# Performance work log

Measured on AMD Instinct MI355X. Metric: run time of the kernel, lower is better.

The kernel has to match this reference:

```python
import jax, jax.numpy as jnp
import numpy as np

N, E, D, L, H = 10000, 160000, 128, 3, 8
DH = D // H
EPS = 1e-5


def ln(x, g, b):
    m = x.mean(-1, keepdims=True)
    v = ((x - m) ** 2).mean(-1, keepdims=True)
    return (x - m) * jax.lax.rsqrt(v + EPS) * g + b


def setup_inputs() -> dict:
    key = jax.random.key(0)
    ks = iter(jax.random.split(key, 16))
    rn = lambda s, sc=0.05: jax.random.normal(next(ks), s, dtype=jnp.float32) * sc
    return {
        'lane_feats': jax.random.normal(next(ks), (N, 10), dtype=jnp.float32),
        'edge_attrs': jax.random.normal(next(ks), (E, 9), dtype=jnp.float32),
        'edge_index': jax.random.randint(next(ks), (2, E), 0, N),
        'node_W': rn((10, D)), 'node_b': jnp.zeros((D,)), 'node_g': jnp.ones((D,)), 'node_bt': jnp.zeros((D,)),
        'rpe_W': rn((9, D)), 'rpe_b': jnp.zeros((D,)), 'rpe_g': jnp.ones((D,)), 'rpe_bt': jnp.zeros((D,)),
        'mem_W': rn((L, 3 * D, D)), 'mem_b': jnp.zeros((L, D)), 'mem_g': jnp.ones((L, D)), 'mem_bt': jnp.zeros((L, D)),
        'Wq': rn((L, D, D)), 'Wk': rn((L, D, D)), 'Wv': rn((L, D, D)), 'Wo': rn((L, D, D)),
        'eu_W': rn((L, D, D)), 'eu_b': jnp.zeros((L, D)), 'eu_g': jnp.ones((L, D)), 'eu_bt': jnp.zeros((L, D)),
        'en_g': jnp.ones((L, D)), 'en_bt': jnp.zeros((L, D)),
        'ffn_W1': rn((L, D, 2 * D)), 'ffn_b1': jnp.zeros((L, 2 * D)),
        'ffn_W2': rn((L, 2 * D, D)), 'ffn_b2': jnp.zeros((L, D)),
        'n1_g': jnp.ones((L, D)), 'n1_bt': jnp.zeros((L, D)),
        'n2_g': jnp.ones((L, D)), 'n2_bt': jnp.zeros((L, D)),
    }


def reference(lane_feats, edge_attrs, edge_index,
              node_W, node_b, node_g, node_bt,
              rpe_W, rpe_b, rpe_g, rpe_bt,
              mem_W, mem_b, mem_g, mem_bt,
              Wq, Wk, Wv, Wo,
              eu_W, eu_b, eu_g, eu_bt,
              en_g, en_bt,
              ffn_W1, ffn_b1, ffn_W2, ffn_b2,
              n1_g, n1_bt, n2_g, n2_bt):
    src, dst = edge_index[0], edge_index[1]
    # input projections (dropout is identity in eval)
    x = jax.nn.relu(ln(lane_feats @ node_W + node_b, node_g, node_bt))  # [N, D]
    e = jax.nn.relu(ln(edge_attrs @ rpe_W + rpe_b, rpe_g, rpe_bt))      # [E, D]
    for l in range(L):
        x_i, x_j = x[dst], x[src]  # receiver / sender features [E, D]
        mem = jax.nn.relu(ln(jnp.concatenate([x_i, x_j, e], axis=-1) @ mem_W[l] + mem_b[l],
                             mem_g[l], mem_bt[l]))
        delta = jax.nn.relu(ln(mem @ eu_W[l] + eu_b[l], eu_g[l], eu_bt[l]))
        e = ln(e + delta, en_g[l], en_bt[l])
        q = (x_i @ Wq[l]).reshape(E, H, DH)
        k = (mem @ Wk[l]).reshape(E, H, DH)
        v = (mem @ Wv[l]).reshape(E, H, DH)
        logits = (q * k).sum(-1) / np.float32(np.sqrt(DH))  # [E, H]
        # segment softmax over destination nodes (pyg_softmax)
        mx = jax.ops.segment_max(logits, dst, num_segments=N)
        ex = jnp.exp(logits - mx[dst])
        sm = jax.ops.segment_sum(ex, dst, num_segments=N)
        attn = ex / (sm[dst] + 1e-16)
        out_e = (attn[..., None] * v).reshape(E, D) @ Wo[l]
        agg = jax.ops.segment_sum(out_e, dst, num_segments=N)  # scatter-add aggregation
        x = ln(x + agg, n1_g[l], n1_bt[l])
        h = jax.nn.relu(x @ ffn_W1[l] + ffn_b1[l]) @ ffn_W2[l] + ffn_b2[l]
        x = ln(x + h, n2_g[l], n2_bt[l])
    return x
```

## Files before the change

### kernel.cpp

```cpp
#include <hip/hip_runtime.h>
#include <cstdint>

#define NN 10000
#define NE 160000
#define DD 128
#define NL 3

typedef __attribute__((ext_vector_type(8))) __bf16 bf16x8;
typedef __attribute__((ext_vector_type(4))) float f32x4;

__device__ __forceinline__ ushort f2bf(float f) {
  unsigned u = __float_as_uint(f);
  return (ushort)((u + 0x7fffu + ((u >> 16) & 1u)) >> 16);
}
__device__ __forceinline__ float bf2f(ushort s) {
  return __uint_as_float(((unsigned)s) << 16);
}
__device__ __forceinline__ float wsum32(float v) {
  v += __shfl_xor(v, 1); v += __shfl_xor(v, 2); v += __shfl_xor(v, 4);
  v += __shfl_xor(v, 8); v += __shfl_xor(v, 16);
  return v;
}
__device__ __forceinline__ float wsum64(float v) {
  v = wsum32(v); v += __shfl_xor(v, 32); return v;
}
__device__ __forceinline__ void red16_2(float& a, float& b) {
#pragma unroll
  for (int m = 1; m < 16; m <<= 1) { a += __shfl_xor(a, m); b += __shfl_xor(b, m); }
}
__device__ __forceinline__ uint4 ldg16(const ushort* p) { return *(const uint4*)p; }

#define PH(id, MAXID, AT, ASTR, KK, AS) {                                       \
    if ((id) < (MAXID)) {                                                       \
      ushort* _db = Bb[((id) + 1) & 1];                                         \
      if ((id) & 1) { *(uint4*)(_db + tid * 8) = sa0;                           \
                      *(uint4*)(_db + 2048 + tid * 8) = sa1; }                  \
      else          { *(uint4*)(_db + tid * 8) = sb0;                           \
                      *(uint4*)(_db + 2048 + tid * 8) = sb1; }                  \
    }                                                                           \
    if ((id) + 2 <= (MAXID)) {                                                  \
      if ((id) & 1) { sb0 = ldg16(csrc((id) + 2, tid));                         \
                      sb1 = ldg16(csrc((id) + 2, 256 + tid)); }                 \
      else          { sa0 = ldg16(csrc((id) + 2, tid));                         \
                      sa1 = ldg16(csrc((id) + 2, 256 + tid)); }                 \
    }                                                                           \
    { bf16x8 _a = *(const bf16x8*)((AT) + (r0 + c) * (ASTR) + (KK) * 32 + g * 8); \
      const ushort* _bp = Bb[(id) & 1] + lane * 8;                              \
      _Pragma("unroll") for (int _t = 0; _t < 8; ++_t)                          \
        AS[_t] = __builtin_amdgcn_mfma_f32_16x16x32_bf16(                       \
            _a, *(const bf16x8*)(_bp + _t * 512), AS[_t], 0, 0, 0); }           \
    __syncthreads(); }

__global__ __launch_bounds__(256) void k_hist(const int* __restrict__ dst,
                                              int* __restrict__ deg) {
  int e = blockIdx.x * 256 + threadIdx.x;
  if (e < NE) atomicAdd(&deg[dst[e]], 1);
}

__global__ __launch_bounds__(256) void k_scan(const int* __restrict__ deg,
                                              int* __restrict__ rowptr,
                                              int* __restrict__ cursor) {
  __shared__ int part[256];
  const int t = threadIdx.x;
  const int CH = 40;
  int base = t * CH;
  int s = 0;
  for (int i = 0; i < CH; ++i) {
    int idx = base + i;
    s += (idx < NN) ? deg[idx] : 0;
  }
  part[t] = s;
  __syncthreads();
  for (int off = 1; off < 256; off <<= 1) {
    int v = (t >= off) ? part[t - off] : 0;
    __syncthreads();
    part[t] += v;
    __syncthreads();
  }
  int run = (t == 0) ? 0 : part[t - 1];
  for (int i = 0; i < CH; ++i) {
    int idx = base + i;
    if (idx < NN) {
      rowptr[idx] = run;
      cursor[idx] = run;
      run += deg[idx];
    }
  }
  if (t == 255) rowptr[NN] = part[255];
}

__global__ __launch_bounds__(256) void k_scatter(const int* __restrict__ dst,
                                                 int* __restrict__ cursor,
                                                 int* __restrict__ eids) {
  int e = blockIdx.x * 256 + threadIdx.x;
  if (e < NE) {
    int pos = atomicAdd(&cursor[dst[e]], 1);
    eids[pos] = e;
  }
}

__global__ __launch_bounds__(256) void k_permidx(const int* __restrict__ ei,
                                                 const int* __restrict__ perm,
                                                 int* __restrict__ srcP,
                                                 int* __restrict__ dstP) {
  int i = blockIdx.x * 256 + threadIdx.x;
  if (i < NE) {
    int e = perm[i];
    srcP[i] = ei[e];
    dstP[i] = ei[NE + e];
  }
}

__global__ __launch_bounds__(256) void k_transp(const float* __restrict__ in,
                                                ushort* __restrict__ out,
                                                int K, int N) {
  __shared__ float T[32][33];
  int k0 = blockIdx.x * 32, n0 = blockIdx.y * 32;
  in += (size_t)blockIdx.z * K * N;
  out += (size_t)blockIdx.z * K * N;
  int tx = threadIdx.x & 31, ty = threadIdx.x >> 5;
#pragma unroll
  for (int r = 0; r < 32; r += 8)
    if (k0 + ty + r < K && n0 + tx < N)
      T[ty + r][tx] = in[(size_t)(k0 + ty + r) * N + n0 + tx];
  __syncthreads();
#pragma unroll
  for (int r = 0; r < 32; r += 8)
    if (n0 + ty + r < N && k0 + tx < K)
      out[(size_t)(n0 + ty + r) * K + k0 + tx] = f2bf(T[tx][ty + r]);
}

template <int K>
__global__ __launch_bounds__(256) void k_inproj(
    const float* __restrict__ inp, const int* __restrict__ perm,
    const float* __restrict__ W, const float* __restrict__ b,
    const float* __restrict__ g, const float* __restrict__ bt,
    float* __restrict__ outF, ushort* __restrict__ outB, int rows) {
  int row = blockIdx.x * 4 + (threadIdx.x >> 6);
  if (row >= rows) return;
  int srow = perm ? perm[row] : row;
  int lane = threadIdx.x & 63;
  float a0 = b[lane], a1 = b[lane + 64];
#pragma unroll
  for (int k = 0; k < K; ++k) {
    float xv = inp[(size_t)srow * K + k];
    a0 = fmaf(xv, W[k * DD + lane], a0);
    a1 = fmaf(xv, W[k * DD + lane + 64], a1);
  }
  float m = wsum64(a0 + a1) * (1.0f / DD);
  float q = wsum64(a0 * a0 + a1 * a1) * (1.0f / DD);
  float rstd = rsqrtf(q - m * m + 1e-5f);
  float o0 = fmaxf((a0 - m) * rstd * g[lane] + bt[lane], 0.0f);
  float o1 = fmaxf((a1 - m) * rstd * g[lane + 64] + bt[lane + 64], 0.0f);
  size_t base = (size_t)row * DD;
  if (outF) { outF[base + lane] = o0; outF[base + lane + 64] = o1; }
  outB[base + lane] = f2bf(o0);
  outB[base + lane + 64] = f2bf(o1);
}

__global__ __launch_bounds__(256) void k_nodepre(
    const ushort* __restrict__ xb, const ushort* __restrict__ memWT,
    const ushort* __restrict__ WqT, const float* __restrict__ memB,
    float* __restrict__ Pa, float* __restrict__ Pb, ushort* __restrict__ qbo) {
  __shared__ __align__(16) ushort Xt[64 * 136];
  __shared__ __align__(16) ushort Bb[4096];
  const int tid = threadIdx.x;
  const int n0 = blockIdx.x * 64;
  const int z = blockIdx.y;
  const ushort* B0 = (z == 0) ? memWT : ((z == 1) ? memWT + 128 : WqT);
  const int bstr = (z < 2) ? 384 : 128;
  uint4 w[2], wn[2];
#pragma unroll
  for (int i = 0; i < 2; ++i) {
    int u = tid + i * 256;
    w[i] = ldg16(B0 + (size_t)(u >> 2) * bstr + (u & 3) * 8);
  }
#pragma unroll
  for (int it = 0; it < 4; ++it) {
    int ch = it * 256 + tid, row = ch >> 4, j = ch & 15;
    int gr = n0 + row; if (gr > NN - 1) gr = NN - 1;
    *(uint4*)(Xt + row * 136 + j * 8) = *(const uint4*)(xb + (size_t)gr * DD + j * 8);
  }
  const int lane = tid & 63, wv = tid >> 6;
  const int c = lane & 15, g = lane >> 4, r0 = wv * 16;
  f32x4 acc[8];
#pragma unroll
  for (int t = 0; t < 8; ++t) acc[t] = (f32x4){0.f, 0.f, 0.f, 0.f};
#pragma unroll
  for (int kk = 0; kk < 4; ++kk) {
    __syncthreads();
#pragma unroll
    for (int i = 0; i < 2; ++i) *(uint4*)(Bb + (tid + i * 256) * 8) = w[i];
    if (kk < 3) {
#pragma unroll
      for (int i = 0; i < 2; ++i) {
        int u = tid + i * 256;
        wn[i] = ldg16(B0 + (size_t)(u >> 2) * bstr + (kk + 1) * 32 + (u & 3) * 8);
      }
    }
    __syncthreads();
    bf16x8 a = *(const bf16x8*)(Xt + (r0 + c) * 136 + kk * 32 + g * 8);
#pragma unroll
    for (int t = 0; t < 8; ++t)
      acc[t] = __builtin_amdgcn_mfma_f32_16x16x32_bf16(
          a, *(const bf16x8*)(Bb + (t * 16 + c) * 32 + g * 8), acc[t], 0, 0, 0);
#pragma unroll
    for (int i = 0; i < 2; ++i) w[i] = wn[i];
  }
  if (z == 0) {
#pragma unroll
    for (int t = 0; t < 8; ++t) {
      float bv = memB[t * 16 + c];
#pragma unroll
      for (int rr = 0; rr < 4; ++rr) {
        int row = n0 + r0 + g * 4 + rr;
        if (row < NN) Pa[(size_t)row * DD + t * 16 + c] = acc[t][rr] + bv;
      }
    }
  } else if (z == 1) {
#pragma unroll
    for (int t = 0; t < 8; ++t)
#pragma unroll
      for (int rr = 0; rr < 4; ++rr) {
        int row = n0 + r0 + g * 4 + rr;
        if (row < NN) Pb[(size_t)row * DD + t * 16 + c] = acc[t][rr];
      }
  } else {
#pragma unroll
    for (int t = 0; t < 8; ++t)
#pragma unroll
      for (int rr = 0; rr < 4; ++rr) {
        int row = n0 + r0 + g * 4 + rr;
        if (row < NN) qbo[(size_t)row * DD + t * 16 + c] = f2bf(acc[t][rr]);
      }
  }
}

__global__ __launch_bounds__(256, 3) void k_edge(
    ushort* __restrict__ ebg, ushort* __restrict__ vbg,
    const float* __restrict__ Pa, const float* __restrict__ Pb,
    const ushort* __restrict__ qb, const int* __restrict__ srcP,
    const int* __restrict__ dstP, const ushort* __restrict__ memWT,
    const float* __restrict__ memG, const float* __restrict__ memBt,
    const ushort* __restrict__ euWT, const float* __restrict__ euB,
    const float* __restrict__ euG, const float* __restrict__ euBt,
    const float* __restrict__ enG, const float* __restrict__ enBt,
    const ushort* __restrict__ WkT, const ushort* __restrict__ WvT,
    float* __restrict__ lg) {
  __shared__ __align__(16) ushort Et[64 * 136];
  __shared__ __align__(16) ushort Mt[64 * 136];
  __shared__ __align__(16) ushort Bb[2][4096];
  const int tid = threadIdx.x;
  const int e0 = blockIdx.x * 64;
  const int lane = tid & 63, wv = tid >> 6;
  const int c = lane & 15, g = lane >> 4, r0 = wv * 16;

  auto csrc = [&](int j, int u) -> const ushort* {
    const ushort* base; int stride, off, kk = j & 3;
    if (j < 4)       { base = memWT; stride = 384; off = 256 + kk * 32; }
    else if (j < 8)  { base = euWT;  stride = 128; off = kk * 32; }
    else if (j < 12) { base = WkT;   stride = 128; off = kk * 32; }
    else             { base = WvT;   stride = 128; off = kk * 32; }
    return base + ((u >> 6) * 16 + (u & 15)) * stride + off + ((u >> 4) & 3) * 8;
  };

  int dv[4], sv[4];
#pragma unroll
  for (int rr = 0; rr < 4; ++rr) {
    int row = e0 + r0 + g * 4 + rr;
    dv[rr] = dstP[row]; sv[rr] = srcP[row];
  }
  uint4 sa0 = ldg16(csrc(0, tid)), sa1 = ldg16(csrc(0, 256 + tid));
  uint4 sb0 = ldg16(csrc(1, tid)), sb1 = ldg16(csrc(1, 256 + tid));
#pragma unroll
  for (int it = 0; it < 4; ++it) {
    int ch = it * 256 + tid, row = ch >> 4, j = ch & 15;
    *(uint4*)(Et + row * 136 + j * 8) =
        *(const uint4*)(ebg + (size_t)(e0 + row) * DD + j * 8);
  }
  *(uint4*)(Bb[0] + tid * 8) = sa0;
  *(uint4*)(Bb[0] + 2048 + tid * 8) = sa1;
  __syncthreads();

  f32x4 acc[8];

#pragma unroll
  for (int t = 0; t < 8; ++t) acc[t] = (f32x4){0.f, 0.f, 0.f, 0.f};
  PH(0, 15, Et, 136, 0, acc)
  PH(1, 15, Et, 136, 1, acc)
  PH(2, 15, Et, 136, 2, acc)
  PH(3, 15, Et, 136, 3, acc)

  {
    float ps[8][4];
#pragma unroll
    for (int t = 0; t < 8; ++t)
#pragma unroll
      for (int rr = 0; rr < 4; ++rr)
        ps[t][rr] = Pa[(size_t)dv[rr] * DD + t * 16 + c] +
                    Pb[(size_t)sv[rr] * DD + t * 16 + c];
    float s1[4] = {0, 0, 0, 0}, s2[4] = {0, 0, 0, 0};
#pragma unroll
    for (int t = 0; t < 8; ++t)
#pragma unroll
      for (int rr = 0; rr < 4; ++rr) {
        float s = acc[t][rr] + ps[t][rr];
        acc[t][rr] = s; s1[rr] += s; s2[rr] += s * s;
      }
    float mean[4], rstd[4];
#pragma unroll
    for (int rr = 0; rr < 4; ++rr) {
      red16_2(s1[rr], s2[rr]);
      mean[rr] = s1[rr] * (1.f / DD);
      rstd[rr] = rsqrtf(s2[rr] * (1.f / DD) - mean[rr] * mean[rr] + 1e-5f);
    }
#pragma unroll
    for (int t = 0; t < 8; ++t) {
      float gv = memG[t * 16 + c], tv = memBt[t * 16 + c];
#pragma unroll
      for (int rr = 0; rr < 4; ++rr) {
        float o = fmaxf((acc[t][rr] - mean[rr]) * rstd[rr] * gv + tv, 0.f);
        Mt[(r0 + g * 4 + rr) * 136 + t * 16 + c] = f2bf(o);
      }
    }
  }
  __syncthreads();

#pragma unroll
  for (int t = 0; t < 8; ++t) acc[t] = (f32x4){0.f, 0.f, 0.f, 0.f};
  PH(4, 15, Mt, 136, 0, acc)
  PH(5, 15, Mt, 136, 1, acc)
  PH(6, 15, Mt, 136, 2, acc)
  PH(7, 15, Mt, 136, 3, acc)

  {
    float s1[4] = {0, 0, 0, 0}, s2[4] = {0, 0, 0, 0};
#pragma unroll
    for (int t = 0; t < 8; ++t) {
      float bv = euB[t * 16 + c];
#pragma unroll
      for (int rr = 0; rr < 4; ++rr) {
        float v2 = acc[t][rr] + bv;
        acc[t][rr] = v2; s1[rr] += v2; s2[rr] += v2 * v2;
      }
    }
    float mean[4], rstd[4];
#pragma unroll
    for (int rr = 0; rr < 4; ++rr) {
      red16_2(s1[rr], s2[rr]);
      mean[rr] = s1[rr] * (1.f / DD);
      rstd[rr] = rsqrtf(s2[rr] * (1.f / DD) - mean[rr] * mean[rr] + 1e-5f);
    }
    float t1[4] = {0, 0, 0, 0}, t2[4] = {0, 0, 0, 0};
#pragma unroll
    for (int t = 0; t < 8; ++t) {
      float gv = euG[t * 16 + c], tv = euBt[t * 16 + c];
#pragma unroll
      for (int rr = 0; rr < 4; ++rr) {
        float d = fmaxf((acc[t][rr] - mean[rr]) * rstd[rr] * gv + tv, 0.f);
        float eo = bf2f(Et[(r0 + g * 4 + rr) * 136 + t * 16 + c]);
        float pv = eo + d;
        acc[t][rr] = pv; t1[rr] += pv; t2[rr] += pv * pv;
      }
    }
    float mean3[4], rstd3[4];
#pragma unroll
    for (int rr = 0; rr < 4; ++rr) {
      red16_2(t1[rr], t2[rr]);
      mean3[rr] = t1[rr] * (1.f / DD);
      rstd3[rr] = rsqrtf(t2[rr] * (1.f / DD) - mean3[rr] * mean3[rr] + 1e-5f);
    }
#pragma unroll
    for (int t = 0; t < 8; ++t) {
      float gv = enG[t * 16 + c], tv = enBt[t * 16 + c];
#pragma unroll
      for (int rr = 0; rr < 4; ++rr) {
        float en = (acc[t][rr] - mean3[rr]) * rstd3[rr] * gv + tv;
        Et[(r0 + g * 4 + rr) * 136 + t * 16 + c] = f2bf(en);
      }
    }
  }
  __syncthreads();
#pragma unroll
  for (int it = 0; it < 4; ++it) {
    int ch = it * 256 + tid, row = ch >> 4, j = ch & 15;
    *(uint4*)(ebg + (size_t)(e0 + row) * DD + j * 8) =
        *(const uint4*)(Et + row * 136 + j * 8);
  }

  float qvf[8][4];
#pragma unroll
  for (int t = 0; t < 8; ++t)
#pragma unroll
    for (int rr = 0; rr < 4; ++rr)
      qvf[t][rr] = bf2f(qb[(size_t)dv[rr] * DD + t * 16 + c]);

#pragma unroll
  for (int t = 0; t < 8; ++t) acc[t] = (f32x4){0.f, 0.f, 0.f, 0.f};
  PH(8, 15, Mt, 136, 0, acc)
  PH(9, 15, Mt, 136, 1, acc)
  PH(10, 15, Mt, 136, 2, acc)
  PH(11, 15, Mt, 136, 3, acc)
#pragma unroll
  for (int t = 0; t < 8; ++t) {
    float p[4];
#pragma unroll
    for (int rr = 0; rr < 4; ++rr) p[rr] = acc[t][rr] * qvf[t][rr];
#pragma unroll
    for (int m = 1; m < 16; m <<= 1)
#pragma unroll
      for (int rr = 0; rr < 4; ++rr) p[rr] += __shfl_xor(p[rr], m);
    if (c == t) {
#pragma unroll
      for (int rr = 0; rr < 4; ++rr)
        lg[(size_t)(e0 + r0 + g * 4 + rr) * 8 + t] = p[rr] * 0.25f;
    }
  }

#pragma unroll
  for (int t = 0; t < 8; ++t) acc[t] = (f32x4){0.f, 0.f, 0.f, 0.f};
  PH(12, 15, Mt, 136, 0, acc)
  PH(13, 15, Mt, 136, 1, acc)
  PH(14, 15, Mt, 136, 2, acc)
  PH(15, 15, Mt, 136, 3, acc)
#pragma unroll
  for (int t = 0; t < 8; ++t)
#pragma unroll
    for (int rr = 0; rr < 4; ++rr)
      Et[(r0 + g * 4 + rr) * 136 + t * 16 + c] = f2bf(acc[t][rr]);
  __syncthreads();
#pragma unroll
  for (int it = 0; it < 4; ++it) {
    int ch = it * 256 + tid, row = ch >> 4, j = ch & 15;
    *(uint4*)(vbg + (size_t)(e0 + row) * DD + j * 8) =
        *(const uint4*)(Et + row * 136 + j * 8);
  }
}

__global__ __launch_bounds__(256) void k_aggr(
    const ushort* __restrict__ vbg, const float* __restrict__ lg,
    const int* __restrict__ rowptr, float* __restrict__ agg) {
  int node = blockIdx.x * 4 + (threadIdx.x >> 6);
  if (node >= NN) return;
  const int lane = threadIdx.x & 63;
  const int j = lane & 7, h = lane >> 3;
  const int beg = rowptr[node], end = rowptr[node + 1];
  float mx = -3.4e38f;
  for (int i = beg + j; i < end; i += 8)
    mx = fmaxf(mx, lg[(size_t)i * 8 + h]);
  mx = fmaxf(mx, __shfl_xor(mx, 1));
  mx = fmaxf(mx, __shfl_xor(mx, 2));
  mx = fmaxf(mx, __shfl_xor(mx, 4));
  float sm = 0.f;
  for (int i = beg + j; i < end; i += 8)
    sm += expf(lg[(size_t)i * 8 + h] - mx);
  sm += __shfl_xor(sm, 1);
  sm += __shfl_xor(sm, 2);
  sm += __shfl_xor(sm, 4);
  float inv = 1.f / (sm + 1e-16f);
  float acc0 = 0.f, acc1 = 0.f;
  for (int i = beg; i < end; ++i) {
    float w = expf(lg[(size_t)i * 8 + h] - mx) * inv;
    ushort2 vv = *(const ushort2*)(vbg + (size_t)i * DD + lane * 2);
    acc0 = fmaf(bf2f(vv.x), w, acc0);
    acc1 = fmaf(bf2f(vv.y), w, acc1);
  }
  *(float2*)(agg + (size_t)node * DD + lane * 2) = make_float2(acc0, acc1);
}

__global__ __launch_bounds__(256) void k_node2(
    const float* __restrict__ vagg, const ushort* __restrict__ WoT,
    const float* __restrict__ xres_g, const float* __restrict__ g1,
    const float* __restrict__ bt1, const ushort* __restrict__ W1T,
    const float* __restrict__ b1, const ushort* __restrict__ W2T,
    const float* __restrict__ b2, const float* __restrict__ g2,
    const float* __restrict__ bt2, float* __restrict__ out,
    ushort* __restrict__ outB) {
  __shared__ __align__(16) ushort Xt[64 * 136];
  __shared__ __align__(16) ushort Hs[64 * 264];
  __shared__ __align__(16) ushort Bb[8192];
  const int tid = threadIdx.x;
  const int n0 = blockIdx.x * 64;
  const int lane = tid & 63, wv = tid >> 6;
  const int c = lane & 15, g = lane >> 4, r0 = wv * 16;

  float xres[8][4];
#pragma unroll
  for (int t = 0; t < 8; ++t)
#pragma unroll
    for (int rr = 0; rr < 4; ++rr) {
      int row = n0 + r0 + g * 4 + rr;
      if (row > NN - 1) row = NN - 1;
      xres[t][rr] = xres_g[(size_t)row * DD + t * 16 + c];
    }
  uint4 w[4], wn[4];
#pragma unroll
  for (int i = 0; i < 2; ++i) {
    int u = tid + i * 256;
    w[i] = ldg16(WoT + (size_t)(u >> 2) * 128 + (u & 3) * 8);
  }
#pragma unroll
  for (int it = 0; it < 8; ++it) {
    int ch = it * 256 + tid, row = ch >> 5, j = ch & 31;
    int gr = n0 + row; if (gr > NN - 1) gr = NN - 1;
    float4 vv = *(const float4*)(vagg + (size_t)gr * DD + j * 4);
    ushort4 ov; ov.x = f2bf(vv.x); ov.y = f2bf(vv.y); ov.z = f2bf(vv.z); ov.w = f2bf(vv.w);
    *(ushort4*)(Xt + row * 136 + j * 4) = ov;
  }
  f32x4 acc0[8];
#pragma unroll
  for (int t = 0; t < 8; ++t) acc0[t] = (f32x4){0.f, 0.f, 0.f, 0.f};
#pragma unroll
  for (int kk = 0; kk < 4; ++kk) {
    __syncthreads();
#pragma unroll
    for (int i = 0; i < 2; ++i) *(uint4*)(Bb + (tid + i * 256) * 8) = w[i];
    if (kk < 3) {
#pragma unroll
      for (int i = 0; i < 2; ++i) {
        int u = tid + i * 256;
        wn[i] = ldg16(WoT + (size_t)(u >> 2) * 128 + (kk + 1) * 32 + (u & 3) * 8);
      }
    }
    __syncthreads();
    bf16x8 a = *(const bf16x8*)(Xt + (r0 + c) * 136 + kk * 32 + g * 8);
#pragma unroll
    for (int t = 0; t < 8; ++t)
      acc0[t] = __builtin_amdgcn_mfma_f32_16x16x32_bf16(
          a, *(const bf16x8*)(Bb + (t * 16 + c) * 32 + g * 8), acc0[t], 0, 0, 0);
#pragma unroll
    for (int i = 0; i < 2; ++i) w[i] = wn[i];
  }
  {
    float s1[4] = {0, 0, 0, 0}, s2[4] = {0, 0, 0, 0};
#pragma unroll
    for (int t = 0; t < 8; ++t)
#pragma unroll
      for (int rr = 0; rr < 4; ++rr) {
        float s = acc0[t][rr] + xres[t][rr];
        acc0[t][rr] = s; s1[rr] += s; s2[rr] += s * s;
      }
    float mean[4], rstd[4];
#pragma unroll
    for (int rr = 0; rr < 4; ++rr) {
      red16_2(s1[rr], s2[rr]);
      mean[rr] = s1[rr] * (1.f / DD);
      rstd[rr] = rsqrtf(s2[rr] * (1.f / DD) - mean[rr] * mean[rr] + 1e-5f);
    }
#pragma unroll
    for (int t = 0; t < 8; ++t) {
      float gv = g1[t * 16 + c], tv = bt1[t * 16 + c];
#pragma unroll
      for (int rr = 0; rr < 4; ++rr) {
        float o = (acc0[t][rr] - mean[rr]) * rstd[rr] * gv + tv;
        Xt[(r0 + g * 4 + rr) * 136 + t * 16 + c] = f2bf(o);
      }
    }
  }
  f32x4 acc16[16];
#pragma unroll
  for (int t = 0; t < 16; ++t) acc16[t] = (f32x4){0.f, 0.f, 0.f, 0.f};
#pragma unroll
  for (int i = 0; i < 4; ++i) {
    int u = tid + i * 256;
    w[i] = ldg16(W1T + (size_t)(u >> 2) * 128 + (u & 3) * 8);
  }
#pragma unroll
  for (int kk = 0; kk < 4; ++kk) {
    __syncthreads();
#pragma unroll
    for (int i = 0; i < 4; ++i) *(uint4*)(Bb + (tid + i * 256) * 8) = w[i];
    if (kk < 3) {
#pragma unroll
      for (int i = 0; i < 4; ++i) {
        int u = tid + i * 256;
        wn[i] = ldg16(W1T + (size_t)(u >> 2) * 128 + (kk + 1) * 32 + (u & 3) * 8);
      }
    }
    __syncthreads();
    bf16x8 a = *(const bf16x8*)(Xt + (r0 + c) * 136 + kk * 32 + g * 8);
#pragma unroll
    for (int t = 0; t < 16; ++t)
      acc16[t] = __builtin_amdgcn_mfma_f32_16x16x32_bf16(
          a, *(const bf16x8*)(Bb + (t * 16 + c) * 32 + g * 8), acc16[t], 0, 0, 0);
#pragma unroll
    for (int i = 0; i < 4; ++i) w[i] = wn[i];
  }
#pragma unroll
  for (int t = 0; t < 16; ++t) {
    float bv = b1[t * 16 + c];
#pragma unroll
    for (int rr = 0; rr < 4; ++rr)
      Hs[(r0 + g * 4 + rr) * 264 + t * 16 + c] = f2bf(fmaxf(acc16[t][rr] + bv, 0.f));
  }
#pragma unroll
  for (int t = 0; t < 8; ++t) acc0[t] = (f32x4){0.f, 0.f, 0.f, 0.f};
#pragma unroll
  for (int i = 0; i < 2; ++i) {
    int u = tid + i * 256;
    w[i] = ldg16(W2T + (size_t)(u >> 2) * 256 + (u & 3) * 8);
  }
#pragma unroll
  for (int kk = 0; kk < 8; ++kk) {
    __syncthreads();
#pragma unroll
    for (int i = 0; i < 2; ++i) *(uint4*)(Bb + (tid + i * 256) * 8) = w[i];
    if (kk < 7) {
#pragma unroll
      for (int i = 0; i < 2; ++i) {
        int u = tid + i * 256;
        wn[i] = ldg16(W2T + (size_t)(u >> 2) * 256 + (kk + 1) * 32 + (u & 3) * 8);
      }
    }
    __syncthreads();
    bf16x8 a = *(const bf16x8*)(Hs + (r0 + c) * 264 + kk * 32 + g * 8);
#pragma unroll
    for (int t = 0; t < 8; ++t)
      acc0[t] = __builtin_amdgcn_mfma_f32_16x16x32_bf16(
          a, *(const bf16x8*)(Bb + (t * 16 + c) * 32 + g * 8), acc0[t], 0, 0, 0);
#pragma unroll
    for (int i = 0; i < 2; ++i) w[i] = wn[i];
  }
  {
    float s1[4] = {0, 0, 0, 0}, s2[4] = {0, 0, 0, 0};
#pragma unroll
    for (int t = 0; t < 8; ++t) {
      float bv = b2[t * 16 + c];
#pragma unroll
      for (int rr = 0; rr < 4; ++rr) {
        float s = acc0[t][rr] + bv + bf2f(Xt[(r0 + g * 4 + rr) * 136 + t * 16 + c]);
        acc0[t][rr] = s; s1[rr] += s; s2[rr] += s * s;
      }
    }
    float mean[4], rstd[4];
#pragma unroll
    for (int rr = 0; rr < 4; ++rr) {
      red16_2(s1[rr], s2[rr]);
      mean[rr] = s1[rr] * (1.f / DD);
      rstd[rr] = rsqrtf(s2[rr] * (1.f / DD) - mean[rr] * mean[rr] + 1e-5f);
    }
#pragma unroll
    for (int t = 0; t < 8; ++t) {
      float gv = g2[t * 16 + c], tv = bt2[t * 16 + c];
#pragma unroll
      for (int rr = 0; rr < 4; ++rr) {
        float o = (acc0[t][rr] - mean[rr]) * rstd[rr] * gv + tv;
        int row = n0 + r0 + g * 4 + rr;
        if (row < NN) out[(size_t)row * DD + t * 16 + c] = o;
        Xt[(r0 + g * 4 + rr) * 136 + t * 16 + c] = f2bf(o);
      }
    }
  }
  __syncthreads();
#pragma unroll
  for (int it = 0; it < 4; ++it) {
    int ch = it * 256 + tid, row = ch >> 4, j = ch & 15;
    int gr = n0 + row;
    if (gr < NN)
      *(uint4*)(outB + (size_t)gr * DD + j * 8) = *(const uint4*)(Xt + row * 136 + j * 8);
  }
}

extern "C" void kernel_launch(void* const* d_in, const int* in_sizes, int n_in,
                              void* d_out, int out_size, void* d_ws,
                              size_t ws_size, hipStream_t stream) {
  (void)in_sizes; (void)n_in; (void)out_size; (void)ws_size;
  const float* lane_feats = (const float*)d_in[0];
  const float* edge_attrs = (const float*)d_in[1];
  const int* ei = (const int*)d_in[2];
  const int* dst = ei + NE;
  const float* node_W = (const float*)d_in[3];
  const float* node_b = (const float*)d_in[4];
  const float* node_g = (const float*)d_in[5];
  const float* node_bt = (const float*)d_in[6];
  const float* rpe_W = (const float*)d_in[7];
  const float* rpe_b = (const float*)d_in[8];
  const float* rpe_g = (const float*)d_in[9];
  const float* rpe_bt = (const float*)d_in[10];
  const float* mem_W = (const float*)d_in[11];
  const float* mem_b = (const float*)d_in[12];
  const float* mem_g = (const float*)d_in[13];
  const float* mem_bt = (const float*)d_in[14];
  const float* Wq = (const float*)d_in[15];
  const float* Wk = (const float*)d_in[16];
  const float* Wv = (const float*)d_in[17];
  const float* Wo = (const float*)d_in[18];
  const float* eu_W = (const float*)d_in[19];
  const float* eu_b = (const float*)d_in[20];
  const float* eu_g = (const float*)d_in[21];
  const float* eu_bt = (const float*)d_in[22];
  const float* en_g = (const float*)d_in[23];
  const float* en_bt = (const float*)d_in[24];
  const float* ffn_W1 = (const float*)d_in[25];
  const float* ffn_b1 = (const float*)d_in[26];
  const float* ffn_W2 = (const float*)d_in[27];
  const float* ffn_b2 = (const float*)d_in[28];
  const float* n1_g = (const float*)d_in[29];
  const float* n1_bt = (const float*)d_in[30];
  const float* n2_g = (const float*)d_in[31];
  const float* n2_bt = (const float*)d_in[32];

  char* p = (char*)d_ws;
  auto alloc = [&](size_t bytes) -> char* {
    char* r = p; p += (bytes + 255) & ~(size_t)255; return r;
  };
  float* x = (float*)alloc((size_t)NN * DD * 4);
  float* vagg = (float*)alloc((size_t)NN * DD * 4);
  float* lg = (float*)alloc((size_t)NE * 8 * 4);
  float* Pa = (float*)alloc((size_t)NN * DD * 4);
  float* Pb = (float*)alloc((size_t)NN * DD * 4);
  ushort* qb = (ushort*)alloc((size_t)NN * DD * 2);
  ushort* xb = (ushort*)alloc((size_t)NN * DD * 2);
  ushort* eb = (ushort*)alloc((size_t)NE * DD * 2);
  ushort* vb = (ushort*)alloc((size_t)NE * DD * 2);
  ushort* memWT = (ushort*)alloc((size_t)NL * DD * 384 * 2);
  ushort* euWT = (ushort*)alloc((size_t)NL * DD * DD * 2);
  ushort* WqT = (ushort*)alloc((size_t)NL * DD * DD * 2);
  ushort* WkT = (ushort*)alloc((size_t)NL * DD * DD * 2);
  ushort* WvT = (ushort*)alloc((size_t)NL * DD * DD * 2);
  ushort* WoT = (ushort*)alloc((size_t)NL * DD * DD * 2);
  ushort* W1T = (ushort*)alloc((size_t)NL * 256 * DD * 2);
  ushort* W2T = (ushort*)alloc((size_t)NL * DD * 256 * 2);
  int* deg = (int*)alloc((size_t)NN * 4);
  int* rowptr = (int*)alloc((size_t)(NN + 1) * 4);
  int* cursor = (int*)alloc((size_t)NN * 4);
  int* eids = (int*)alloc((size_t)NE * 4);
  int* srcP = (int*)alloc((size_t)NE * 4);
  int* dstP = (int*)alloc((size_t)NE * 4);

  hipMemsetAsync(deg, 0, (size_t)NN * 4, stream);
  k_hist<<<NE / 256, 256, 0, stream>>>(dst, deg);
  k_scan<<<1, 256, 0, stream>>>(deg, rowptr, cursor);
  k_scatter<<<NE / 256, 256, 0, stream>>>(dst, cursor, eids);
  k_permidx<<<NE / 256, 256, 0, stream>>>(ei, eids, srcP, dstP);

  k_transp<<<dim3(12, 4, NL), 256, 0, stream>>>(mem_W, memWT, 384, DD);
  k_transp<<<dim3(4, 4, NL), 256, 0, stream>>>(eu_W, euWT, DD, DD);
  k_transp<<<dim3(4, 4, NL), 256, 0, stream>>>(Wq, WqT, DD, DD);
  k_transp<<<dim3(4, 4, NL), 256, 0, stream>>>(Wk, WkT, DD, DD);
  k_transp<<<dim3(4, 4, NL), 256, 0, stream>>>(Wv, WvT, DD, DD);
  k_transp<<<dim3(4, 4, NL), 256, 0, stream>>>(Wo, WoT, DD, DD);
  k_transp<<<dim3(4, 8, NL), 256, 0, stream>>>(ffn_W1, W1T, DD, 256);
  k_transp<<<dim3(8, 4, NL), 256, 0, stream>>>(ffn_W2, W2T, 256, DD);

  k_inproj<10><<<NN / 4, 256, 0, stream>>>(lane_feats, nullptr, node_W, node_b,
                                           node_g, node_bt, x, xb, NN);
  k_inproj<9><<<NE / 4, 256, 0, stream>>>(edge_attrs, eids, rpe_W, rpe_b,
                                          rpe_g, rpe_bt, nullptr, eb, NE);

  const int NB = (NN + 63) / 64;
  for (int l = 0; l < NL; ++l) {
    k_nodepre<<<dim3(NB, 3), 256, 0, stream>>>(
        xb, memWT + (size_t)l * DD * 384, WqT + (size_t)l * DD * DD,
        mem_b + l * DD, Pa, Pb, qb);
    k_edge<<<NE / 64, 256, 0, stream>>>(
        eb, vb, Pa, Pb, qb, srcP, dstP, memWT + (size_t)l * DD * 384,
        mem_g + l * DD, mem_bt + l * DD, euWT + (size_t)l * DD * DD,
        eu_b + l * DD, eu_g + l * DD, eu_bt + l * DD, en_g + l * DD,
        en_bt + l * DD, WkT + (size_t)l * DD * DD, WvT + (size_t)l * DD * DD,
        lg);
    k_aggr<<<(NN + 3) / 4, 256, 0, stream>>>(vb, lg, rowptr, vagg);
    k_node2<<<NB, 256, 0, stream>>>(
        vagg, WoT + (size_t)l * DD * DD, x, n1_g + l * DD, n1_bt + l * DD,
        W1T + (size_t)l * 256 * DD, ffn_b1 + l * 256,
        W2T + (size_t)l * DD * 256, ffn_b2 + l * DD, n2_g + l * DD,
        n2_bt + l * DD, (l == NL - 1) ? (float*)d_out : x, xb);
  }
}
```

Measured before the change: 522.3 us.

## Batch weight transposes, cache softmax exponentials, raise MFMA wave priority

```diff
diff --git a/kernel.cpp b/kernel.cpp
--- a/kernel.cpp
+++ b/kernel.cpp
@@ -46,9 +46,11 @@
     }                                                                           \
     { bf16x8 _a = *(const bf16x8*)((AT) + (r0 + c) * (ASTR) + (KK) * 32 + g * 8); \
       const ushort* _bp = Bb[(id) & 1] + lane * 8;                              \
+      __builtin_amdgcn_s_setprio(1);                                            \
       _Pragma("unroll") for (int _t = 0; _t < 8; ++_t)                          \
         AS[_t] = __builtin_amdgcn_mfma_f32_16x16x32_bf16(                       \
-            _a, *(const bf16x8*)(_bp + _t * 512), AS[_t], 0, 0, 0); }           \
+            _a, *(const bf16x8*)(_bp + _t * 512), AS[_t], 0, 0, 0);             \
+      __builtin_amdgcn_s_setprio(0); }                                          \
     __syncthreads(); }
 
 __global__ __launch_bounds__(256) void k_hist(const int* __restrict__ dst,
@@ -128,6 +130,31 @@
   for (int r = 0; r < 32; r += 8)
     if (n0 + ty + r < N && k0 + tx < K)
       out[(size_t)(n0 + ty + r) * K + k0 + tx] = f2bf(T[tx][ty + r]);
+}
+
+__global__ __launch_bounds__(256) void k_transp5(
+    const float* __restrict__ Wa, const float* __restrict__ Wb,
+    const float* __restrict__ Wc, const float* __restrict__ Wd,
+    const float* __restrict__ We, ushort* __restrict__ Oa,
+    ushort* __restrict__ Ob, ushort* __restrict__ Oc, ushort* __restrict__ Od,
+    ushort* __restrict__ Oe) {
+  __shared__ float T[32][33];
+  int l = blockIdx.z / 5, wsel = blockIdx.z % 5;
+  const float* in =
+      (wsel == 0 ? Wa : wsel == 1 ? Wb : wsel == 2 ? Wc : wsel == 3 ? Wd : We) +
+      (size_t)l * 128 * 128;
+  ushort* out =
+      (wsel == 0 ? Oa : wsel == 1 ? Ob : wsel == 2 ? Oc : wsel == 3 ? Od : Oe) +
+      (size_t)l * 128 * 128;
+  int k0 = blockIdx.x * 32, n0 = blockIdx.y * 32;
+  int tx = threadIdx.x & 31, ty = threadIdx.x >> 5;
+#pragma unroll
+  for (int r = 0; r < 32; r += 8)
+    T[ty + r][tx] = in[(size_t)(k0 + ty + r) * 128 + n0 + tx];
+  __syncthreads();
+#pragma unroll
+  for (int r = 0; r < 32; r += 8)
+    out[(size_t)(n0 + ty + r) * 128 + k0 + tx] = f2bf(T[tx][ty + r]);
 }
 
 template <int K>
@@ -438,7 +465,7 @@
 }
 
 __global__ __launch_bounds__(256) void k_aggr(
-    const ushort* __restrict__ vbg, const float* __restrict__ lg,
+    const ushort* __restrict__ vbg, float* __restrict__ lg,
     const int* __restrict__ rowptr, float* __restrict__ agg) {
   int node = blockIdx.x * 4 + (threadIdx.x >> 6);
   if (node >= NN) return;
@@ -452,15 +479,19 @@
   mx = fmaxf(mx, __shfl_xor(mx, 2));
   mx = fmaxf(mx, __shfl_xor(mx, 4));
   float sm = 0.f;
-  for (int i = beg + j; i < end; i += 8)
-    sm += expf(lg[(size_t)i * 8 + h] - mx);
+  for (int i = beg + j; i < end; i += 8) {
+    float ex = expf(lg[(size_t)i * 8 + h] - mx);
+    lg[(size_t)i * 8 + h] = ex;
+    sm += ex;
+  }
   sm += __shfl_xor(sm, 1);
   sm += __shfl_xor(sm, 2);
   sm += __shfl_xor(sm, 4);
   float inv = 1.f / (sm + 1e-16f);
+  asm volatile("s_waitcnt vmcnt(0)" ::: "memory");
   float acc0 = 0.f, acc1 = 0.f;
   for (int i = beg; i < end; ++i) {
-    float w = expf(lg[(size_t)i * 8 + h] - mx) * inv;
+    float w = lg[(size_t)i * 8 + h] * inv;
     ushort2 vv = *(const ushort2*)(vbg + (size_t)i * DD + lane * 2);
     acc0 = fmaf(bf2f(vv.x), w, acc0);
     acc1 = fmaf(bf2f(vv.y), w, acc1);
@@ -735,11 +766,8 @@
   k_permidx<<<NE / 256, 256, 0, stream>>>(ei, eids, srcP, dstP);
 
   k_transp<<<dim3(12, 4, NL), 256, 0, stream>>>(mem_W, memWT, 384, DD);
-  k_transp<<<dim3(4, 4, NL), 256, 0, stream>>>(eu_W, euWT, DD, DD);
-  k_transp<<<dim3(4, 4, NL), 256, 0, stream>>>(Wq, WqT, DD, DD);
-  k_transp<<<dim3(4, 4, NL), 256, 0, stream>>>(Wk, WkT, DD, DD);
-  k_transp<<<dim3(4, 4, NL), 256, 0, stream>>>(Wv, WvT, DD, DD);
-  k_transp<<<dim3(4, 4, NL), 256, 0, stream>>>(Wo, WoT, DD, DD);
+  k_transp5<<<dim3(4, 4, 5 * NL), 256, 0, stream>>>(
+      Wq, Wk, Wv, Wo, eu_W, WqT, WkT, WvT, WoT, euWT);
   k_transp<<<dim3(4, 8, NL), 256, 0, stream>>>(ffn_W1, W1T, DD, 256);
   k_transp<<<dim3(8, 4, NL), 256, 0, stream>>>(ffn_W2, W2T, 256, DD);
 
```

New measurement: 509.2 us, median of 3. 1.03x faster.
